# Kernel tuning notes

Measured on AMD Instinct MI355X. Metric: run time of the kernel, lower is better.

The kernel has to match this reference:

```python
import jax, jax.numpy as jnp
import numpy as np

B, D, L, K = 8, 256, 2048, 24
R = L // 2 + 1  # rfft bins
H = 2 * D      # mlp hidden
EPS = 1e-5


def setup_inputs() -> dict:
    key = jax.random.key(0)
    ks = jax.random.split(key, 10)
    s_theta = 1.0 / np.sqrt(D)   # ~kaiming_uniform scale
    s_w1 = 1.0 / np.sqrt(D)
    s_w2 = 1.0 / np.sqrt(H)
    return {
        "x": jax.random.normal(ks[0], (B, D, L), dtype=jnp.float32),
        "Phi_f_re": jax.random.normal(ks[1], (K, R), dtype=jnp.float32),
        "Phi_f_im": jax.random.normal(ks[2], (K, R), dtype=jnp.float32),
        "Theta": jax.random.uniform(ks[3], (K, D, D), jnp.float32, -s_theta, s_theta),
        "gamma": jnp.ones((D,), jnp.float32),
        "beta": jnp.zeros((D,), jnp.float32),
        "W1": jax.random.uniform(ks[4], (H, D), jnp.float32, -s_w1, s_w1),
        "b1": jax.random.uniform(ks[5], (H,), jnp.float32, -s_w1, s_w1),
        "W2": jax.random.uniform(ks[6], (D, H), jnp.float32, -s_w2, s_w2),
        "b2": jax.random.uniform(ks[7], (D,), jnp.float32, -s_w2, s_w2),
    }


def reference(x, Phi_f_re, Phi_f_im, Theta, gamma, beta, W1, b1, W2, b2):
    # x: [B, D, L]. LayerNorm over channel dim D (torch norms last dim of x.transpose(1,2)).
    mu = jnp.mean(x, axis=1, keepdims=True)
    var = jnp.var(x, axis=1, keepdims=True)
    z = (x - mu) * jax.lax.rsqrt(var + EPS) * gamma[None, :, None] + beta[None, :, None]

    Xf = jnp.fft.rfft(z, axis=-1)                       # [B, D, R] complex
    Phi_c = Phi_f_re - 1j * Phi_f_im                    # conj(Phi_f), [K, R]
    # Sf[b,h,r] = sum_{d,k} Xf[b,d,r] * conj(Phi)[k,r] * Theta[k,h,d]
    # (identical to the torch real/imag split since Theta is real)
    Sf = jnp.einsum('bdr,kr,khd->bhr', Xf, Phi_c, Theta)
    S = jnp.fft.irfft(Sf, n=L, axis=-1)                 # [B, D, L]

    # 1x1 Conv1d MLP with exact GELU
    h = jax.nn.gelu(jnp.einsum('hd,bdl->bhl', W1, S) + b1[None, :, None], approximate=False)
    out = jnp.einsum('dh,bhl->bdl', W2, h) + b2[None, :, None]
    return x + out
```

## Files before the change

kernel.cpp:

```cpp
#include <hip/hip_runtime.h>
#include <hip/hip_bf16.h>
#include <hip/hip_fp16.h>
#include <math.h>

#define BB 8
#define DD 256
#define LL 2048
#define KK 24
#define RR 1025
#define HH 512

typedef __attribute__((ext_vector_type(8))) _Float16 f16x8;
typedef __attribute__((ext_vector_type(4))) float f32x4;

__device__ __forceinline__ unsigned short f2h(float f) {
  return __builtin_bit_cast(unsigned short, __float2half_rn(f));
}

__global__ void ln_kernel(const float* __restrict__ x, const float* __restrict__ gamma,
                          const float* __restrict__ beta, float* __restrict__ z) {
  __shared__ float red[2][4][64];
  __shared__ float mu_s[64], rs_s[64];
  int blk = blockIdx.x;
  int b = blk >> 5;
  int l0 = (blk & 31) << 6;
  int t = threadIdx.x;
  int ll = t & 63;
  int part = t >> 6;
  int l = l0 + ll;
  const float* xb = x + ((size_t)b * DD) * LL + l;
  float xv[64];
  float s = 0.f, ss = 0.f;
  #pragma unroll
  for (int i = 0; i < 64; ++i) {
    float v = xb[(size_t)(part * 64 + i) * LL];
    xv[i] = v; s += v; ss += v * v;
  }
  red[0][part][ll] = s; red[1][part][ll] = ss;
  __syncthreads();
  if (part == 0) {
    float S = red[0][0][ll] + red[0][1][ll] + red[0][2][ll] + red[0][3][ll];
    float Q = red[1][0][ll] + red[1][1][ll] + red[1][2][ll] + red[1][3][ll];
    float mu = S * (1.f / 256.f);
    float var = Q * (1.f / 256.f) - mu * mu;
    mu_s[ll] = mu; rs_s[ll] = rsqrtf(var + 1e-5f);
  }
  __syncthreads();
  float mu = mu_s[ll], rs = rs_s[ll];
  float* zb = z + ((size_t)b * DD) * LL + l;
  #pragma unroll
  for (int i = 0; i < 64; ++i) {
    int d = part * 64 + i;
    zb[(size_t)d * LL] = (xv[i] - mu) * rs * gamma[d] + beta[d];
  }
}

__global__ void theta_prep(const float* __restrict__ Theta, unsigned* __restrict__ A2u) {
  int bi = blockIdx.x;
  int k = bi >> 8, h = bi & 255;
  int t = threadIdx.x;
  float2 v = *reinterpret_cast<const float2*>(Theta + (size_t)k * 65536 + h * 256 + 2 * t);
  A2u[(size_t)h * 3072 + k * 128 + t] =
      __builtin_bit_cast(unsigned, __floats2half2_rn(v.x, v.y));
}

__global__ void w_prep(const float* __restrict__ W1, const float* __restrict__ W2,
                       unsigned* __restrict__ W1h, unsigned* __restrict__ W2h) {
  int i = blockIdx.x * 256 + threadIdx.x;
  float2 a = reinterpret_cast<const float2*>(W1)[i];
  W1h[i] = __builtin_bit_cast(unsigned, __floats2half2_rn(a.x, a.y));
  float2 b = reinterpret_cast<const float2*>(W2)[i];
  W2h[i] = __builtin_bit_cast(unsigned, __floats2half2_rn(b.x, b.y));
}

__device__ __forceinline__ float2* fft2048(float2* bufA, float2* bufB,
                                           const float2* __restrict__ tw, int t) {
  float2* src = bufA; float2* dst = bufB;
  for (int stage = 0; stage < 11; ++stage) {
    int s = 1 << stage;
    #pragma unroll
    for (int j = 0; j < 4; ++j) {
      int idx = t + 256 * j;
      int q = idx & (s - 1);
      int p = idx >> stage;
      float2 a = src[idx];
      float2 b = src[idx + 1024];
      float sr = a.x + b.x, si = a.y + b.y;
      float dr = a.x - b.x, di = a.y - b.y;
      float2 w = tw[p << stage];
      dst[q + 2 * s * p] = make_float2(sr, si);
      dst[q + 2 * s * p + s] = make_float2(dr * w.x - di * w.y, dr * w.y + di * w.x);
    }
    __syncthreads();
    float2* tmp = src; src = dst; dst = tmp;
  }
  return src;
}

__device__ __forceinline__ void build_tw(float2* tw, int t) {
  #pragma unroll
  for (int j = 0; j < 4; ++j) {
    int i = t + 256 * j;
    float xfrac = (float)i * (1.f / 1024.f);
    tw[i] = make_float2(cospif(xfrac), -sinpif(xfrac));
  }
}

__global__ void rfft_kernel(const float* __restrict__ z, unsigned* __restrict__ Xf2) {
  __shared__ float2 bufA[2048];
  __shared__ float2 bufB[2048];
  __shared__ float2 tw[1024];
  int row = blockIdx.x;
  int t = threadIdx.x;
  build_tw(tw, t);
  const float* zr = z + (size_t)row * LL;
  #pragma unroll
  for (int j = 0; j < 8; ++j) {
    int i = t + 256 * j;
    bufA[i] = make_float2(zr[i], 0.f);
  }
  __syncthreads();
  float2* res = fft2048(bufA, bufB, tw, t);
  #pragma unroll
  for (int j = 0; j < 5; ++j) {
    int r = t + 256 * j;
    if (r <= 1024) {
      float2 v = res[r];
      Xf2[(size_t)row * RR + r] = __builtin_bit_cast(unsigned, __floats2half2_rn(v.x, v.y));
    }
  }
}

__global__ void irfft_kernel(const float2* __restrict__ Sf, float* __restrict__ S) {
  __shared__ float2 bufA[2048];
  __shared__ float2 bufB[2048];
  __shared__ float2 tw[1024];
  int row = blockIdx.x;
  int t = threadIdx.x;
  build_tw(tw, t);
  const float2* fr = Sf + (size_t)row * RR;
  #pragma unroll
  for (int j = 0; j < 8; ++j) {
    int i = t + 256 * j;
    float2 v;
    if (i <= 1024) { v = fr[i]; v.y = -v.y; }
    else           { v = fr[2048 - i]; }
    bufA[i] = v;
  }
  __syncthreads();
  float2* res = fft2048(bufA, bufB, tw, t);
  const float scale = 1.f / 2048.f;
  float* sr = S + (size_t)row * LL;
  #pragma unroll
  for (int j = 0; j < 8; ++j) {
    int i = t + 256 * j;
    sr[i] = res[i].x * scale;
  }
}

__global__ void __launch_bounds__(256)
spectral_mfma(const unsigned* __restrict__ Xf2,
              const unsigned short* __restrict__ A2,
              const float* __restrict__ Phi_re,
              const float* __restrict__ Phi_im,
              float2* __restrict__ Sf) {
  __shared__ unsigned xs_r[32][35];
  __shared__ unsigned xs_i[32][35];
  __shared__ alignas(16) unsigned Bl[2][64][68];
  __shared__ unsigned phi_pr[KK][4], phi_pi[KK][4];

  int t = threadIdx.x;
  int lane = t & 63;
  int w = t >> 6;
  int l15 = lane & 15;
  int l4 = lane >> 4;
  int r0 = blockIdx.x << 2;
  int h0 = blockIdx.y << 7;

  int bc = t & 31;
  int rq = t >> 5;
  int rl_b = rq >> 1;

  if (t < 96) {
    int k = t >> 2, rl = t & 3;
    int rc = min(r0 + rl, RR - 1);
    float pr = Phi_re[k * RR + rc], pi = Phi_im[k * RR + rc];
    phi_pr[k][rl] = __builtin_bit_cast(unsigned, __floats2half2_rn(pr, pr));
    phi_pi[k][rl] = __builtin_bit_cast(unsigned, __floats2half2_rn(pi, pi));
  }

  f32x4 acc[2][4];
  #pragma unroll
  for (int fm = 0; fm < 2; ++fm)
    #pragma unroll
    for (int fn = 0; fn < 4; ++fn) acc[fm][fn] = (f32x4){0.f, 0.f, 0.f, 0.f};

  const unsigned short* Arow0 = A2 + (size_t)(h0 + w * 32 + l15) * 6144 + l4 * 8;
  const unsigned short* Arow1 = Arow0 + (size_t)16 * 6144;

  #define SPEC_BUILD128(kk2, bbuf)                                             \
    {                                                                          \
      _Pragma("unroll")                                                        \
      for (int j_ = 0; j_ < 8; j_ += 2) {                                      \
        int b_ = ((rq & 1) << 2) + (j_ >> 1);                                  \
        unsigned xr_ = xs_r[bc][rl_b * 8 + b_];                                \
        unsigned xi_ = xs_i[bc][rl_b * 8 + b_];                                \
        __half2 xrh_ = __builtin_bit_cast(__half2, xr_);                       \
        __half2 xih_ = __builtin_bit_cast(__half2, xi_);                       \
        _Pragma("unroll")                                                      \
        for (int p_ = 0; p_ < 2; ++p_) {                                       \
          __half2 pr_ = __builtin_bit_cast(__half2, phi_pr[(kk2) + p_][rl_b]); \
          __half2 pi_ = __builtin_bit_cast(__half2, phi_pi[(kk2) + p_][rl_b]); \
          __half2 re_ = __hfma2(xrh_, pr_, __hmul2(xih_, pi_));                \
          __half2 im_ = __hfma2(xih_, pr_, __hneg2(__hmul2(xrh_, pi_)));       \
          Bl[bbuf][rq * 8 + j_][p_ * 32 + bc] = __builtin_bit_cast(unsigned, re_); \
          Bl[bbuf][rq * 8 + j_ + 1][p_ * 32 + bc] = __builtin_bit_cast(unsigned, im_); \
        }                                                                      \
      }                                                                        \
    }

  for (int win = 0; win < 4; ++win) {
    __syncthreads();
    #pragma unroll
    for (int e = 0; e < 4; ++e) {
      int idx = t + 256 * e;
      int d2 = idx >> 5;
      int r8b = idx & 31;
      int rl = r8b >> 3, b = r8b & 7;
      int d = win * 64 + 2 * d2;
      int rc = min(r0 + rl, RR - 1);
      unsigned u0 = Xf2[(size_t)(b * DD + d) * RR + rc];
      unsigned u1 = Xf2[(size_t)(b * DD + d + 1) * RR + rc];
      xs_r[d2][r8b] = (u0 & 0xffffu) | (u1 << 16);
      xs_i[d2][r8b] = (u0 >> 16) | (u1 & 0xffff0000u);
    }
    __syncthreads();
    SPEC_BUILD128(0, 0);
    __syncthreads();
    for (int ph = 0; ph < 12; ++ph) {
      const int buf = ph & 1;
      if (ph < 11) SPEC_BUILD128(2 * (ph + 1), buf ^ 1);
      #pragma unroll
      for (int ks = 0; ks < 4; ++ks) {
        size_t kcol = (size_t)(2 * ph + (ks >> 1)) * 256 + win * 64 + (ks & 1) * 32;
        f16x8 a0 = *reinterpret_cast<const f16x8*>(Arow0 + kcol);
        f16x8 a1 = *reinterpret_cast<const f16x8*>(Arow1 + kcol);
        #pragma unroll
        for (int fn = 0; fn < 4; ++fn) {
          f16x8 bf = *reinterpret_cast<const f16x8*>(
              &Bl[buf][fn * 16 + l15][ks * 16 + l4 * 4]);
          acc[0][fn] = __builtin_amdgcn_mfma_f32_16x16x32_f16(a0, bf, acc[0][fn], 0, 0, 0);
          acc[1][fn] = __builtin_amdgcn_mfma_f32_16x16x32_f16(a1, bf, acc[1][fn], 0, 0, 0);
        }
      }
      __syncthreads();
    }
  }

  float* Sff = reinterpret_cast<float*>(Sf);
  int b = l15 >> 1, ri = l15 & 1;
  #pragma unroll
  for (int fm = 0; fm < 2; ++fm)
    #pragma unroll
    for (int fn = 0; fn < 4; ++fn) {
      int r = min(r0 + fn, RR - 1);
      #pragma unroll
      for (int i = 0; i < 4; ++i) {
        int h = h0 + w * 32 + fm * 16 + l4 * 4 + i;
        Sff[((((size_t)(b * DD + h)) * RR + r) << 1) + ri] = acc[fm][fn][i];
      }
    }
  #undef SPEC_BUILD128
}

__global__ void __launch_bounds__(256)
mlp_mfma(const float* __restrict__ S, const float* __restrict__ x,
         const unsigned short* __restrict__ W1h,
         const float* __restrict__ b1,
         const unsigned short* __restrict__ W2h,
         const float* __restrict__ b2,
         float* __restrict__ out) {
  __shared__ unsigned short S_lds[64 * 256];
  __shared__ unsigned short H_lds[64 * 128];
  char* Sb = reinterpret_cast<char*>(S_lds);
  char* Hb = reinterpret_cast<char*>(H_lds);

  int t = threadIdx.x;
  int lane = t & 63, w = t >> 6;
  int l15 = lane & 15, l4 = lane >> 4;
  int bb = blockIdx.x >> 5;
  int l0 = (blockIdx.x & 31) << 6;

  {
    int n = t & 63;
    int dbase = t >> 6;
    int n7s = (n & 7) << 4;
    const float* Sp = S + ((size_t)(bb * DD)) * LL + l0 + n;
    #pragma unroll 8
    for (int p = 0; p < 64; ++p) {
      int d = p * 4 + dbase;
      float v = Sp[(size_t)d * LL];
      *reinterpret_cast<unsigned short*>(Sb + n * 512 + ((2 * d) ^ n7s)) = f2h(v);
    }
  }

  f32x4 acc2[4][4];
  #pragma unroll
  for (int fm = 0; fm < 4; ++fm)
    #pragma unroll
    for (int fn = 0; fn < 4; ++fn) acc2[fm][fn] = (f32x4){0.f, 0.f, 0.f, 0.f};

  for (int ch = 0; ch < 4; ++ch) {
    __syncthreads();
    f32x4 acc1[2][4];
    #pragma unroll
    for (int fm = 0; fm < 2; ++fm) {
      float4 b1v = *reinterpret_cast<const float4*>(
          b1 + ch * 128 + w * 32 + fm * 16 + l4 * 4);
      #pragma unroll
      for (int fn = 0; fn < 4; ++fn)
        acc1[fm][fn] = (f32x4){b1v.x, b1v.y, b1v.z, b1v.w};
    }
    #pragma unroll
    for (int ks = 0; ks < 8; ++ks) {
      f16x8 af0 = *reinterpret_cast<const f16x8*>(
          W1h + (size_t)(ch * 128 + w * 32 + l15) * 256 + ks * 32 + l4 * 8);
      f16x8 af1 = *reinterpret_cast<const f16x8*>(
          W1h + (size_t)(ch * 128 + w * 32 + 16 + l15) * 256 + ks * 32 + l4 * 8);
      #pragma unroll
      for (int fn = 0; fn < 4; ++fn) {
        int n = fn * 16 + l15;
        f16x8 bf = *reinterpret_cast<const f16x8*>(
            Sb + n * 512 + ((64 * ks + 16 * l4) ^ ((n & 7) << 4)));
        acc1[0][fn] = __builtin_amdgcn_mfma_f32_16x16x32_f16(af0, bf, acc1[0][fn], 0, 0, 0);
        acc1[1][fn] = __builtin_amdgcn_mfma_f32_16x16x32_f16(af1, bf, acc1[1][fn], 0, 0, 0);
      }
    }
    #pragma unroll
    for (int fm = 0; fm < 2; ++fm)
      #pragma unroll
      for (int fn = 0; fn < 4; ++fn) {
        unsigned short hv[4];
        #pragma unroll
        for (int i = 0; i < 4; ++i) {
          float v = acc1[fm][fn][i];
          hv[i] = f2h(0.5f * v * (1.f + erff(v * 0.70710678118654752f)));
        }
        int n = fn * 16 + l15;
        int hl2 = 2 * (w * 32 + fm * 16 + l4 * 4);
        *reinterpret_cast<uint2*>(Hb + n * 256 + (hl2 ^ ((n & 7) << 4))) =
            *reinterpret_cast<uint2*>(hv);
      }
    __syncthreads();
    #pragma unroll
    for (int ks = 0; ks < 4; ++ks) {
      f16x8 bfv[4];
      #pragma unroll
      for (int fn = 0; fn < 4; ++fn) {
        int n = fn * 16 + l15;
        bfv[fn] = *reinterpret_cast<const f16x8*>(
            Hb + n * 256 + ((64 * ks + 16 * l4) ^ ((n & 7) << 4)));
      }
      #pragma unroll
      for (int fm = 0; fm < 4; ++fm) {
        f16x8 af = *reinterpret_cast<const f16x8*>(
            W2h + (size_t)(w * 64 + fm * 16 + l15) * 512 + ch * 128 + ks * 32 + l4 * 8);
        #pragma unroll
        for (int fn = 0; fn < 4; ++fn)
          acc2[fm][fn] = __builtin_amdgcn_mfma_f32_16x16x32_f16(af, bfv[fn], acc2[fm][fn], 0, 0, 0);
      }
    }
  }

  #pragma unroll
  for (int fm = 0; fm < 4; ++fm) {
    float4 b2v = *reinterpret_cast<const float4*>(b2 + w * 64 + fm * 16 + l4 * 4);
    #pragma unroll
    for (int i = 0; i < 4; ++i) {
      int d = w * 64 + fm * 16 + l4 * 4 + i;
      const float* xr = x + ((size_t)(bb * DD + d)) * LL + l0;
      float* orow = out + ((size_t)(bb * DD + d)) * LL + l0;
      float bias = (i == 0) ? b2v.x : (i == 1) ? b2v.y : (i == 2) ? b2v.z : b2v.w;
      #pragma unroll
      for (int fn = 0; fn < 4; ++fn) {
        int n = fn * 16 + l15;
        orow[n] = xr[n] + bias + acc2[fm][fn][i];
      }
    }
  }
}

extern "C" void kernel_launch(void* const* d_in, const int* in_sizes, int n_in,
                              void* d_out, int out_size, void* d_ws, size_t ws_size,
                              hipStream_t stream) {
  const float* x      = (const float*)d_in[0];
  const float* Phi_re = (const float*)d_in[1];
  const float* Phi_im = (const float*)d_in[2];
  const float* Theta  = (const float*)d_in[3];
  const float* gamma  = (const float*)d_in[4];
  const float* beta   = (const float*)d_in[5];
  const float* W1     = (const float*)d_in[6];
  const float* b1     = (const float*)d_in[7];
  const float* W2     = (const float*)d_in[8];
  const float* b2     = (const float*)d_in[9];

  float* ws = (float*)d_ws;
  float*    z   = ws;
  unsigned* Xf2 = (unsigned*)(ws + 4194304);
  float2*   Sf  = (float2*)(ws + 8392704);
  unsigned* A2u = (unsigned*)(ws + 12591104);
  unsigned* W1h = (unsigned*)(ws + 14163968);
  unsigned* W2h = (unsigned*)(ws + 14295040);

  ln_kernel<<<dim3(BB * (LL / 64)), 256, 0, stream>>>(x, gamma, beta, z);
  theta_prep<<<dim3(KK * 256), 128, 0, stream>>>(Theta, A2u);
  w_prep<<<dim3(256), 256, 0, stream>>>(W1, W2, W1h, W2h);
  rfft_kernel<<<dim3(BB * DD), 256, 0, stream>>>(z, Xf2);
  spectral_mfma<<<dim3(257, 2), 256, 0, stream>>>(
      Xf2, (const unsigned short*)A2u, Phi_re, Phi_im, Sf);
  irfft_kernel<<<dim3(BB * DD), 256, 0, stream>>>(Sf, z);
  mlp_mfma<<<dim3(256), 256, 0, stream>>>(
      z, x, (const unsigned short*)W1h, b1, (const unsigned short*)W2h, b2,
      (float*)d_out);
}
```

Measured before the change: 261.3 us.

## Transpose spectral input and output so spectral GEMM accesses are coalesced

Adds two tiled transpose kernels. One reorders the packed rfft output to a frequency-major layout before the spectral MFMA kernel, and the other reorders the spectral result back to row-major for the irfft. The spectral kernel now loads contiguous uint2 pairs and writes contiguous 16-float groups, replacing the strided gathers and scatters across rows of length 1025. This trades uncoalesced access inside the GEMM for two extra full passes over the spectra and two more kernel launches, and it reshuffles workspace offsets.

Measured after the change: 250.5 us. 1.04x faster.

```diff
diff --git a/kernel.cpp b/kernel.cpp
--- a/kernel.cpp
+++ b/kernel.cpp
@@ -71,6 +71,43 @@
   W1h[i] = __builtin_bit_cast(unsigned, __floats2half2_rn(a.x, a.y));
   float2 b = reinterpret_cast<const float2*>(W2)[i];
   W2h[i] = __builtin_bit_cast(unsigned, __floats2half2_rn(b.x, b.y));
+}
+
+__global__ void xpose_xf(const unsigned* __restrict__ in, unsigned* __restrict__ out) {
+  __shared__ unsigned tile[32][33];
+  int c0 = blockIdx.x * 32;
+  int r0 = blockIdx.y * 32;
+  int tx = threadIdx.x, ty = threadIdx.y;
+  for (int i = ty; i < 32; i += 8) {
+    int c = c0 + tx;
+    tile[i][tx] = (c < RR) ? in[(size_t)(r0 + i) * RR + c] : 0u;
+  }
+  __syncthreads();
+  for (int i = ty; i < 32; i += 8) {
+    int c = c0 + i;
+    if (c < RR) out[(size_t)c * 2048 + r0 + tx] = tile[tx][i];
+  }
+}
+
+__global__ void xpose_sf(const float* __restrict__ in, float2* __restrict__ out) {
+  __shared__ float tile[32][33];
+  int r0 = blockIdx.x * 32;
+  int c0 = blockIdx.y * 32;
+  int tx = threadIdx.x, ty = threadIdx.y;
+  for (int i = ty; i < 32; i += 8) {
+    int r = r0 + i;
+    tile[i][tx] = (r < RR) ? in[(size_t)r * 4096 + c0 + tx] : 0.f;
+  }
+  __syncthreads();
+  int r = r0 + tx;
+  if (r < RR) {
+    for (int p = ty; p < 16; p += 8) {
+      int hn = c0 + 2 * p;
+      int h = hn >> 4, n = hn & 15;
+      int bh = (n >> 1) * 256 + h;
+      out[(size_t)bh * RR + r] = make_float2(tile[tx][2 * p], tile[tx][2 * p + 1]);
+    }
+  }
 }
 
 __device__ __forceinline__ float2* fft2048(float2* bufA, float2* bufB,
@@ -159,11 +196,11 @@
 }
 
 __global__ void __launch_bounds__(256)
-spectral_mfma(const unsigned* __restrict__ Xf2,
+spectral_mfma(const unsigned* __restrict__ Xf2T,
               const unsigned short* __restrict__ A2,
               const float* __restrict__ Phi_re,
               const float* __restrict__ Phi_im,
-              float2* __restrict__ Sf) {
+              float* __restrict__ SfT) {
   __shared__ unsigned xs_r[32][35];
   __shared__ unsigned xs_i[32][35];
   __shared__ alignas(16) unsigned Bl[2][64][68];
@@ -224,15 +261,14 @@
     #pragma unroll
     for (int e = 0; e < 4; ++e) {
       int idx = t + 256 * e;
-      int d2 = idx >> 5;
-      int r8b = idx & 31;
-      int rl = r8b >> 3, b = r8b & 7;
-      int d = win * 64 + 2 * d2;
+      int rl = idx >> 8;
+      int b  = (idx >> 5) & 7;
+      int d2 = idx & 31;
       int rc = min(r0 + rl, RR - 1);
-      unsigned u0 = Xf2[(size_t)(b * DD + d) * RR + rc];
-      unsigned u1 = Xf2[(size_t)(b * DD + d + 1) * RR + rc];
-      xs_r[d2][r8b] = (u0 & 0xffffu) | (u1 << 16);
-      xs_i[d2][r8b] = (u0 >> 16) | (u1 & 0xffff0000u);
+      const uint2 u = *reinterpret_cast<const uint2*>(
+          Xf2T + (size_t)rc * 2048 + b * 256 + win * 64 + 2 * d2);
+      xs_r[d2][rl * 8 + b] = (u.x & 0xffffu) | (u.y << 16);
+      xs_i[d2][rl * 8 + b] = (u.x >> 16) | (u.y & 0xffff0000u);
     }
     __syncthreads();
     SPEC_BUILD128(0, 0);
@@ -257,8 +293,6 @@
     }
   }
 
-  float* Sff = reinterpret_cast<float*>(Sf);
-  int b = l15 >> 1, ri = l15 & 1;
   #pragma unroll
   for (int fm = 0; fm < 2; ++fm)
     #pragma unroll
@@ -267,7 +301,7 @@
       #pragma unroll
       for (int i = 0; i < 4; ++i) {
         int h = h0 + w * 32 + fm * 16 + l4 * 4 + i;
-        Sff[((((size_t)(b * DD + h)) * RR + r) << 1) + ri] = acc[fm][fn][i];
+        SfT[((size_t)r * 256 + h) * 16 + l15] = acc[fm][fn][i];
       }
     }
   #undef SPEC_BUILD128
@@ -405,20 +439,24 @@
   const float* b2     = (const float*)d_in[9];
 
   float* ws = (float*)d_ws;
-  float*    z   = ws;
-  unsigned* Xf2 = (unsigned*)(ws + 4194304);
-  float2*   Sf  = (float2*)(ws + 8392704);
-  unsigned* A2u = (unsigned*)(ws + 12591104);
-  unsigned* W1h = (unsigned*)(ws + 14163968);
-  unsigned* W2h = (unsigned*)(ws + 14295040);
+  float*    z    = ws;
+  unsigned* Xf2  = (unsigned*)(ws + 4194304);
+  unsigned* Xf2T = (unsigned*)(ws + 6293504);
+  float*    SfT  = ws + 8392704;
+  float2*   SfN  = (float2*)(ws + 4194304);
+  unsigned* A2u  = (unsigned*)(ws + 12591104);
+  unsigned* W1h  = (unsigned*)(ws + 13377536);
+  unsigned* W2h  = (unsigned*)(ws + 13443072);
 
   ln_kernel<<<dim3(BB * (LL / 64)), 256, 0, stream>>>(x, gamma, beta, z);
   theta_prep<<<dim3(KK * 256), 128, 0, stream>>>(Theta, A2u);
   w_prep<<<dim3(256), 256, 0, stream>>>(W1, W2, W1h, W2h);
   rfft_kernel<<<dim3(BB * DD), 256, 0, stream>>>(z, Xf2);
+  xpose_xf<<<dim3(33, 64), dim3(32, 8), 0, stream>>>(Xf2, Xf2T);
   spectral_mfma<<<dim3(257, 2), 256, 0, stream>>>(
-      Xf2, (const unsigned short*)A2u, Phi_re, Phi_im, Sf);
-  irfft_kernel<<<dim3(BB * DD), 256, 0, stream>>>(Sf, z);
+      Xf2T, (const unsigned short*)A2u, Phi_re, Phi_im, SfT);
+  xpose_sf<<<dim3(33, 128), dim3(32, 8), 0, stream>>>(SfT, SfN);
+  irfft_kernel<<<dim3(BB * DD), 256, 0, stream>>>(SfN, z);
   mlp_mfma<<<dim3(256), 256, 0, stream>>>(
       z, x, (const unsigned short*)W1h, b1, (const unsigned short*)W2h, b2,
       (float*)d_out);
```
